# Optimization experiments

Hardware: AMD Instinct MI355X
Metric: run time of the kernel (lower is better)

Reference implementation:

```python
import jax, jax.numpy as jnp
import numpy as np

B, L = 4, 2048
D_MODEL = 1024
D_INNER = 2048      # expand * d_model
D_STATE = 16
D_CONV = 4
DT_RANK = 64        # ceil(d_model / 16)
EPS = 1e-5


def setup_inputs() -> dict:
    key = jax.random.key(0)
    ks = jax.random.split(key, 8)
    s = 0.02
    return {
        "x": jax.random.normal(ks[0], (B, L, D_MODEL), jnp.float32),
        "ln1_g": jnp.ones((D_MODEL,), jnp.float32),
        "ln1_b": jnp.zeros((D_MODEL,), jnp.float32),
        "ln2_g": jnp.ones((D_MODEL,), jnp.float32),
        "ln2_b": jnp.zeros((D_MODEL,), jnp.float32),
        "in_proj_w": jax.random.normal(ks[1], (D_MODEL, 2 * D_INNER), jnp.float32) * s,
        "conv_w": jax.random.normal(ks[2], (D_INNER, D_CONV), jnp.float32) * s,
        "conv_b": jnp.zeros((D_INNER,), jnp.float32),
        "x_proj_w": jax.random.normal(ks[3], (D_INNER, DT_RANK + 2 * D_STATE), jnp.float32) * s,
        "dt_proj_w": jax.random.normal(ks[4], (DT_RANK, D_INNER), jnp.float32) * s,
        # softplus^{-1}(0.01): mamba-style dt bias init
        "dt_proj_b": jnp.log(jnp.expm1(jnp.full((D_INNER,), 0.01, jnp.float32))),
        "A_log": jnp.log(jnp.broadcast_to(jnp.arange(1, D_STATE + 1, dtype=jnp.float32), (D_INNER, D_STATE))),
        "Dp": jnp.ones((D_INNER,), jnp.float32),
        "out_proj_w": jax.random.normal(ks[5], (D_INNER, D_MODEL), jnp.float32) * s,
        "mlp_w": jax.random.normal(ks[6], (D_MODEL, D_MODEL), jnp.float32) * s,
        "mlp_b": jnp.zeros((D_MODEL,), jnp.float32),
    }


def _layernorm(x, g, b):
    mu = jnp.mean(x, axis=-1, keepdims=True)
    var = jnp.mean(jnp.square(x - mu), axis=-1, keepdims=True)
    return (x - mu) * jax.lax.rsqrt(var + EPS) * g + b


def _mamba(x, in_proj_w, conv_w, conv_b, x_proj_w, dt_proj_w, dt_proj_b, A_log, Dp, out_proj_w):
    # x: (B, L, d_model)
    xz = x @ in_proj_w                       # (B, L, 2*d_inner)
    u, z = jnp.split(xz, 2, axis=-1)         # each (B, L, d_inner)

    # depthwise causal conv1d, kernel width D_CONV
    up = jnp.pad(u, ((0, 0), (D_CONV - 1, 0), (0, 0)))
    uc = conv_b
    for k in range(D_CONV):
        uc = uc + up[:, k:k + L, :] * conv_w[:, k]
    u = jax.nn.silu(uc)                      # (B, L, d_inner)

    dbc = u @ x_proj_w                       # (B, L, dt_rank + 2*d_state)
    dt = dbc[..., :DT_RANK]
    Bm = dbc[..., DT_RANK:DT_RANK + D_STATE]  # (B, L, d_state)
    Cm = dbc[..., DT_RANK + D_STATE:]         # (B, L, d_state)
    delta = jax.nn.softplus(dt @ dt_proj_w + dt_proj_b)  # (B, L, d_inner)
    A = -jnp.exp(A_log)                      # (d_inner, d_state)

    def step(h, inp):
        u_t, d_t, B_t, C_t = inp             # (B,d_inner),(B,d_inner),(B,d_state),(B,d_state)
        dA = jnp.exp(d_t[:, :, None] * A)    # (B, d_inner, d_state)
        h = dA * h + (d_t * u_t)[:, :, None] * B_t[:, None, :]
        y = jnp.einsum('bds,bs->bd', h, C_t)
        return h, y

    h0 = jnp.zeros((x.shape[0], D_INNER, D_STATE), x.dtype)
    xs = (u.transpose(1, 0, 2), delta.transpose(1, 0, 2),
          Bm.transpose(1, 0, 2), Cm.transpose(1, 0, 2))
    _, ys = jax.lax.scan(step, h0, xs)       # ys: (L, B, d_inner)
    y = ys.transpose(1, 0, 2) + u * Dp
    y = y * jax.nn.silu(z)
    return y @ out_proj_w                    # (B, L, d_model)


def reference(x, ln1_g, ln1_b, ln2_g, ln2_b, in_proj_w, conv_w, conv_b,
              x_proj_w, dt_proj_w, dt_proj_b, A_log, Dp, out_proj_w, mlp_w, mlp_b):
    h = _layernorm(x, ln1_g, ln1_b)
    h = _mamba(h, in_proj_w, conv_w, conv_b, x_proj_w, dt_proj_w, dt_proj_b,
               A_log, Dp, out_proj_w)
    # residual=False -> x = x_ssm; stage 2: Linear + GELU (exact erf)
    h2 = _layernorm(h, ln2_g, ln2_b)
    out = jax.nn.gelu(h2 @ mlp_w + mlp_b, approximate=False)
    return out
```

## Files before the change

### kernel.cpp

```cpp
#include <hip/hip_runtime.h>
#include <hip/hip_bf16.h>
#include <math.h>

#define BB 4
#define LL 2048
#define DM 1024
#define DI 2048
#define DS 16
#define DC 4
#define DTR 64

#define NCH 8
#define TC  (LL / NCH)

typedef __hip_bfloat16 bf16;
typedef unsigned int u32;
typedef unsigned short u16;
typedef u16 u16x8 __attribute__((ext_vector_type(8)));
typedef u16 u16x4 __attribute__((ext_vector_type(4)));
typedef short short8 __attribute__((ext_vector_type(8)));
typedef float f32x4 __attribute__((ext_vector_type(4)));

__device__ __forceinline__ float bfb2f(u16 b) { return __uint_as_float(((u32)b) << 16); }
__device__ __forceinline__ u16 f2bfb(float f) {
  bf16 h = __float2bfloat16(f);
  u16 r; __builtin_memcpy(&r, &h, 2); return r;
}

__device__ __forceinline__ float xld(const void* p, size_t i, bool isbf) {
  return isbf ? __bfloat162float(((const bf16*)p)[i]) : ((const float*)p)[i];
}
__device__ __forceinline__ bool probe_bf(const u32* probe) {
  return probe[0] == 0x3F803F80u;
}

__device__ __forceinline__ float softplus_f(float x) {
  return fmaxf(x, 0.f) + __logf(1.f + __expf(-fabsf(x)));
}
__device__ __forceinline__ float gelu_f(float x) {
  return 0.5f * x * (1.f + erff(x * 0.70710678118654752440f));
}
__device__ __forceinline__ float silu_f(float x) {
  return x * __builtin_amdgcn_rcpf(1.f + __expf(-x));
}

template<int PAT>
__device__ __forceinline__ float swz_xor(float v) {
  return __uint_as_float(
      (u32)__builtin_amdgcn_ds_swizzle((int)__float_as_uint(v), PAT));
}
template<int CTRL>
__device__ __forceinline__ float dpp_xchg(float v) {
  return __uint_as_float((u32)__builtin_amdgcn_update_dpp(
      0, (int)__float_as_uint(v), CTRL, 0xF, 0xF, true));
}

__device__ __forceinline__ float block_sum(float v, float* sm) {
  #pragma unroll
  for (int o = 32; o > 0; o >>= 1) v += __shfl_down(v, o, 64);
  int w = threadIdx.x >> 6;
  __syncthreads();
  if ((threadIdx.x & 63) == 0) sm[w] = v;
  __syncthreads();
  return sm[0] + sm[1] + sm[2] + sm[3];
}

template<bool EXT>
__global__ __launch_bounds__(256)
void ln_kernel(const void* __restrict__ X, const void* __restrict__ g,
               const void* __restrict__ bvec, bf16* __restrict__ Y,
               const u32* __restrict__ probe) {
  __shared__ float sm[4];
  bool isbf = probe_bf(probe);
  int row = blockIdx.x;
  int tid = threadIdx.x;
  size_t base = (size_t)row * DM;
  float v[4];
  float s = 0.f;
  #pragma unroll
  for (int i = 0; i < 4; i++) {
    int c = tid + 256 * i;
    v[i] = EXT ? xld(X, base + c, isbf) : ((const float*)X)[base + c];
    s += v[i];
  }
  float mu = block_sum(s, sm) * (1.f / DM);
  float vs = 0.f;
  #pragma unroll
  for (int i = 0; i < 4; i++) { float d = v[i] - mu; vs += d * d; }
  float var = block_sum(vs, sm) * (1.f / DM);
  float inv = rsqrtf(var + 1e-5f);
  bf16* yr = Y + base;
  #pragma unroll
  for (int i = 0; i < 4; i++) {
    int c = tid + 256 * i;
    yr[c] = __float2bfloat16((v[i] - mu) * inv * xld(g, c, isbf) + xld(bvec, c, isbf));
  }
}

__global__ __launch_bounds__(256)
void transpose_w(const void* __restrict__ W, u16* __restrict__ WT,
                 int K, int N, const u32* __restrict__ probe) {
  __shared__ u16 tile[32][33];
  bool isbf = probe_bf(probe);
  int c = threadIdx.x & 31;
  int r0 = threadIdx.x >> 5;
  int n0 = blockIdx.x * 32;
  int k0 = blockIdx.y * 32;
  #pragma unroll
  for (int rr = 0; rr < 32; rr += 8) {
    int r = r0 + rr;
    tile[r][c] = f2bfb(xld(W, (size_t)(k0 + r) * N + n0 + c, isbf));
  }
  __syncthreads();
  #pragma unroll
  for (int rr = 0; rr < 32; rr += 8) {
    int r = r0 + rr;
    WT[(size_t)(n0 + r) * K + k0 + c] = tile[c][r];
  }
}

__global__ __launch_bounds__(256)
void transpose_y(const u16* __restrict__ src, u16* __restrict__ dst) {
  __shared__ u16 tile[32][33];
  const size_t PER_B = (size_t)DI * LL;
  int b = blockIdx.z;
  int t0 = blockIdx.x * 32;
  int d0 = blockIdx.y * 32;
  int c = threadIdx.x & 31;
  int r0 = threadIdx.x >> 5;
  #pragma unroll
  for (int rr = 0; rr < 32; rr += 8) {
    int r = r0 + rr;
    tile[r][c] = src[b * PER_B + (size_t)(d0 + r) * LL + t0 + c];
  }
  __syncthreads();
  #pragma unroll
  for (int rr = 0; rr < 32; rr += 8) {
    int r = r0 + rr;
    dst[b * PER_B + (size_t)(t0 + r) * DI + d0 + c] = tile[c][r];
  }
}

template<int EPI>
__global__ __launch_bounds__(256)
void gemm_mfma(const u16* __restrict__ A, int lda,
               const u16* __restrict__ BT,
               const void* __restrict__ bias,
               void* __restrict__ C0, void* __restrict__ C1, void* __restrict__ C2,
               int N, int K, int ldc,
               const u32* __restrict__ probe) {
  __shared__ u16 As[128][40];
  __shared__ u16 Bs[128][40];
  bool isbf = probe_bf(probe);
  int tid = threadIdx.x;
  int wave = tid >> 6;
  int lane = tid & 63;
  int wm = wave >> 1, wn = wave & 1;
  int quad = lane >> 4;
  int l15 = lane & 15;
  int m0 = blockIdx.y * 128;
  int n0 = blockIdx.x * 128;

  f32x4 acc[4][4] = {};

  int sr = tid >> 2;
  int scc = tid & 3;

  for (int k0 = 0; k0 < K; k0 += 32) {
    *(u16x8*)(&As[sr][scc * 8]) =
        *(const u16x8*)(A + (size_t)(m0 + sr) * lda + k0 + scc * 8);
    *(u16x8*)(&As[64 + sr][scc * 8]) =
        *(const u16x8*)(A + (size_t)(m0 + 64 + sr) * lda + k0 + scc * 8);
    *(u16x8*)(&Bs[sr][scc * 8]) =
        *(const u16x8*)(BT + (size_t)(n0 + sr) * K + k0 + scc * 8);
    *(u16x8*)(&Bs[64 + sr][scc * 8]) =
        *(const u16x8*)(BT + (size_t)(n0 + 64 + sr) * K + k0 + scc * 8);
    __syncthreads();
    short8 af[4], bf[4];
    #pragma unroll
    for (int i = 0; i < 4; i++) {
      af[i] = *(const short8*)(&As[wm * 64 + i * 16 + l15][quad * 8]);
      bf[i] = *(const short8*)(&Bs[wn * 64 + i * 16 + l15][quad * 8]);
    }
    #pragma unroll
    for (int i = 0; i < 4; i++)
      #pragma unroll
      for (int j = 0; j < 4; j++)
        acc[i][j] = __builtin_amdgcn_mfma_f32_16x16x32_bf16(af[i], bf[j], acc[i][j], 0, 0, 0);
    __syncthreads();
  }

  #pragma unroll
  for (int i = 0; i < 4; i++) {
    int rb = m0 + wm * 64 + i * 16 + quad * 4;
    #pragma unroll
    for (int j = 0; j < 4; j++) {
      int c = n0 + wn * 64 + j * 16 + l15;
      if (EPI == 0) {
        #pragma unroll
        for (int r = 0; r < 4; r++)
          ((float*)C0)[(size_t)(rb + r) * ldc + c] = acc[i][j][r];
      } else if (EPI == 2) {
        float bv = xld(bias, c, isbf);
        #pragma unroll
        for (int r = 0; r < 4; r++) {
          float v = gelu_f(acc[i][j][r] + bv);
          if (isbf) ((bf16*)C0)[(size_t)(rb + r) * ldc + c] = __float2bfloat16(v);
          else      ((float*)C0)[(size_t)(rb + r) * ldc + c] = v;
        }
      } else if (EPI == 3) {
        int b = rb >> 11;
        int t = rb & (LL - 1);
        u16x4 pk;
        #pragma unroll
        for (int r = 0; r < 4; r++) pk[r] = f2bfb(acc[i][j][r]);
        u16* dst = (c < DI) ? (u16*)C0 : (u16*)C1;
        int cc = (c < DI) ? c : c - DI;
        *(u16x4*)(dst + ((size_t)b * DI + cc) * LL + t) = pk;
      } else {
        int b = rb >> 11;
        int t = rb & (LL - 1);
        if (c < DTR) {
          #pragma unroll
          for (int r = 0; r < 4; r++)
            ((float*)C0)[(size_t)(rb + r) * DTR + c] = acc[i][j][r];
        } else if (c < DTR + 2 * DS) {
          float* dst = (c < DTR + DS) ? (float*)C1 : (float*)C2;
          int s = (c < DTR + DS) ? c - DTR : c - DTR - DS;
          float* p = dst + (((size_t)b * (LL / 8) + (t >> 3)) * DS + s) * 8 + (t & 7);
          #pragma unroll
          for (int r = 0; r < 4; r++) p[r] = acc[i][j][r];
        }
      }
    }
  }
}

__global__ __launch_bounds__(256)
void gemm_dtproj(const float* __restrict__ A, int lda,
                 const void* __restrict__ Bw, int ldb,
                 const void* __restrict__ bias,
                 u16* __restrict__ C0, int N, int K,
                 const u32* __restrict__ probe) {
  __shared__ float As[16][65];
  __shared__ float Bs[16][65];
  bool isbf = probe_bf(probe);
  int tid = threadIdx.x;
  int tx = tid & 15, ty = tid >> 4;
  int m0 = blockIdx.y * 64;
  int n0 = blockIdx.x * 64;
  float acc[4][4] = {};
  int arow = tid >> 2;
  int akq = (tid & 3) * 4;
  int bk = tid >> 4;
  int bcq = (tid & 15) * 4;

  for (int k0 = 0; k0 < K; k0 += 16) {
    const float* ap = A + (size_t)(m0 + arow) * lda + k0 + akq;
    #pragma unroll
    for (int i = 0; i < 4; i++) As[akq + i][arow] = ap[i];
    size_t boff = (size_t)(k0 + bk) * ldb + n0 + bcq;
    #pragma unroll
    for (int j = 0; j < 4; j++) Bs[bk][bcq + j] = xld(Bw, boff + j, isbf);
    __syncthreads();
    #pragma unroll
    for (int k = 0; k < 16; k++) {
      float a4[4], b4[4];
      #pragma unroll
      for (int i = 0; i < 4; i++) a4[i] = As[k][ty + 16 * i];
      #pragma unroll
      for (int j = 0; j < 4; j++) b4[j] = Bs[k][tx + 16 * j];
      #pragma unroll
      for (int i = 0; i < 4; i++)
        #pragma unroll
        for (int j = 0; j < 4; j++)
          acc[i][j] = fmaf(a4[i], b4[j], acc[i][j]);
    }
    __syncthreads();
  }
  #pragma unroll
  for (int i = 0; i < 4; i++) {
    int r = m0 + ty + 16 * i;
    int t = r & (LL - 1);
    int b = r >> 11;
    #pragma unroll
    for (int j = 0; j < 4; j++) {
      int c = n0 + tx + 16 * j;
      float sv = softplus_f(acc[i][j] + xld(bias, c, isbf));
      C0[((size_t)b * DI + c) * LL + t] = f2bfb(sv);
    }
  }
}

__global__ __launch_bounds__(256)
void conv_kernel(const u16* __restrict__ uT, const void* __restrict__ cw,
                 const void* __restrict__ cb, u16* __restrict__ ucT,
                 const u32* __restrict__ probe) {
  bool isbf = probe_bf(probe);
  size_t pos = ((size_t)blockIdx.x * 256 + threadIdx.x) * 8;
  int t0 = (int)(pos & (LL - 1));
  int d = (int)((pos >> 11) & (DI - 1));
  float w0 = xld(cw, d * DC + 0, isbf);
  float w1 = xld(cw, d * DC + 1, isbf);
  float w2 = xld(cw, d * DC + 2, isbf);
  float w3 = xld(cw, d * DC + 3, isbf);
  float bias = xld(cb, d, isbf);
  u16x8 cur = *(const u16x8*)(uT + pos);
  float u[11];
  if (t0 > 0) {
    u16x4 prev = *(const u16x4*)(uT + pos - 4);
    u[0] = bfb2f(prev[1]); u[1] = bfb2f(prev[2]); u[2] = bfb2f(prev[3]);
  } else {
    u[0] = 0.f; u[1] = 0.f; u[2] = 0.f;
  }
  #pragma unroll
  for (int i = 0; i < 8; i++) u[3 + i] = bfb2f(cur[i]);
  u16x8 out;
  #pragma unroll
  for (int i = 0; i < 8; i++) {
    float acc = bias + w0 * u[i] + w1 * u[i + 1] + w2 * u[i + 2] + w3 * u[i + 3];
    out[i] = f2bfb(silu_f(acc));
  }
  *(u16x8*)(ucT + pos) = out;
}

__global__ __launch_bounds__(256)
void scan_fused(const u16* __restrict__ zT, u16* __restrict__ ucT,
                const u16* __restrict__ deltaT,
                const float* __restrict__ Bt, const float* __restrict__ Ct,
                const void* __restrict__ A_log, const void* __restrict__ Dp,
                const u32* __restrict__ probe) {
  __shared__ float sP[2][NCH][DS];
  __shared__ float sH[2][NCH][DS];
  bool isbf = probe_bf(probe);
  int tid = threadIdx.x;
  int s = tid & 15;
  int chunk = (tid >> 4) & (NCH - 1);
  int cl = tid >> 7;
  int chain = blockIdx.x * 2 + cl;
  int b = chain >> 11;
  int d = chain & (DI - 1);

  float a = -__expf(xld(A_log, d * DS + s, isbf));
  const u16* dl = deltaT + ((size_t)b * DI + d) * LL + chunk * TC;
  const u16* up = ucT    + ((size_t)b * DI + d) * LL + chunk * TC;
  const float* bp = Bt + (((size_t)b * (LL / 8) + (chunk * TC >> 3)) * DS + s) * 8;

  float P = 1.f, Q = 0.f;
  for (int t0 = 0; t0 < TC; t0 += 8) {
    u16x8 dt8 = *(const u16x8*)(dl + t0);
    u16x8 u8  = *(const u16x8*)(up + t0);
    float4 b4a = *(const float4*)(bp + t0 * 16);
    float4 b4b = *(const float4*)(bp + t0 * 16 + 4);
    float Bv[8] = {b4a.x, b4a.y, b4a.z, b4a.w, b4b.x, b4b.y, b4b.z, b4b.w};
    #pragma unroll
    for (int i = 0; i < 8; i++) {
      float dt = bfb2f(dt8[i]);
      float uv = bfb2f(u8[i]);
      float dA = __expf(dt * a);
      Q = fmaf(dA, Q, dt * uv * Bv[i]);
      P *= dA;
    }
  }
  sP[cl][chunk][s] = P;
  sH[cl][chunk][s] = Q;
  __syncthreads();
  if (tid < 32) {
    int ci = tid >> 4, ss = tid & 15;
    float carry = 0.f;
    #pragma unroll
    for (int c = 0; c < NCH; c++) {
      float nxt = sP[ci][c][ss] * carry + sH[ci][c][ss];
      sH[ci][c][ss] = carry;
      carry = nxt;
    }
  }
  __syncthreads();
  float h = sH[cl][chunk][s];

  float dp = xld(Dp, d, isbf);
  const float* cp = Ct + (((size_t)b * (LL / 8) + (chunk * TC >> 3)) * DS + s) * 8;
  const u16* zp = zT  + ((size_t)b * DI + d) * LL + chunk * TC;
  u16* upw = ucT      + ((size_t)b * DI + d) * LL + chunk * TC;
  bool k8 = (s & 8) != 0;
  bool k1 = (s & 1) != 0;
  bool k4 = (s & 4) != 0;
  int ei = ((s >> 3) & 1) * 4 + (s & 1) * 2 + ((s >> 2) & 1);
  bool estore = (s & 2) == 0;

  for (int t0 = 0; t0 < TC; t0 += 8) {
    u16x8 dt8 = *(const u16x8*)(dl + t0);
    u16x8 u8  = *(const u16x8*)(up + t0);
    float4 b4a = *(const float4*)(bp + t0 * 16);
    float4 b4b = *(const float4*)(bp + t0 * 16 + 4);
    float4 c4a = *(const float4*)(cp + t0 * 16);
    float4 c4b = *(const float4*)(cp + t0 * 16 + 4);
    float Bv[8] = {b4a.x, b4a.y, b4a.z, b4a.w, b4b.x, b4b.y, b4b.z, b4b.w};
    float Cv[8] = {c4a.x, c4a.y, c4a.z, c4a.w, c4b.x, c4b.y, c4b.z, c4b.w};
    float v[8];
    #pragma unroll
    for (int i = 0; i < 8; i++) {
      float dt = bfb2f(dt8[i]);
      float uv = bfb2f(u8[i]);
      float dA = __expf(dt * a);
      h = fmaf(dA, h, dt * uv * Bv[i]);
      v[i] = h * Cv[i];
    }
    float w4[4];
    #pragma unroll
    for (int j = 0; j < 4; j++) {
      float lo = v[j], hi = v[j + 4];
      float snd = k8 ? lo : hi;
      float kp  = k8 ? hi : lo;
      w4[j] = kp + dpp_xchg<0x128>(snd);
    }
    float w2[2];
    #pragma unroll
    for (int k = 0; k < 2; k++) {
      float lo = w4[k], hi = w4[k + 2];
      float snd = k1 ? lo : hi;
      float kp  = k1 ? hi : lo;
      w2[k] = kp + dpp_xchg<0xB1>(snd);
    }
    float y1;
    {
      float lo = w2[0], hi = w2[1];
      float snd = k4 ? lo : hi;
      float kp  = k4 ? hi : lo;
      y1 = kp + swz_xor<0x101F>(snd);
    }
    y1 += dpp_xchg<0x4E>(y1);
    int t = t0 + ei;
    float uvs = bfb2f(up[t]);
    float zvs = bfb2f(zp[t]);
    float val = fmaf(uvs, dp, y1) * silu_f(zvs);
    if (estore) upw[t] = f2bfb(val);
  }
}

extern "C" void kernel_launch(void* const* d_in, const int* in_sizes, int n_in,
                              void* d_out, int out_size, void* d_ws, size_t ws_size,
                              hipStream_t stream) {
  const void* x         = d_in[0];
  const u32*  probe     = (const u32*)d_in[1];
  const void* ln1_g     = d_in[1];
  const void* ln1_b     = d_in[2];
  const void* ln2_g     = d_in[3];
  const void* ln2_b     = d_in[4];
  const void* in_proj_w = d_in[5];
  const void* conv_w    = d_in[6];
  const void* conv_b    = d_in[7];
  const void* x_proj_w  = d_in[8];
  const void* dt_proj_w = d_in[9];
  const void* dt_proj_b = d_in[10];
  const void* A_log     = d_in[11];
  const void* Dp        = d_in[12];
  const void* out_proj_w= d_in[13];
  const void* mlp_w     = d_in[14];
  const void* mlp_b     = d_in[15];

  const size_t MB = 1024 * 1024;
  char* ws = (char*)d_ws;
  bf16*  h1       = (bf16*)(ws + 0);
  u16*   opwT     = (u16*)(ws + 0);
  bf16*  h2       = (bf16*)(ws + 0);
  u16*   xpwT     = (u16*)(ws + 4 * MB);
  u16*   uT       = (u16*)(ws + 16 * MB);
  u16*   uc2      = uT;
  u16*   deltaT   = uT;
  u16*   y        = uT;
  u16*   zT       = (u16*)(ws + 48 * MB);
  float* o        = (float*)(ws + 48 * MB);
  u16*   ipwT     = (u16*)(ws + 80 * MB);
  u16*   ucT      = (u16*)(ws + 80 * MB);
  u16*   mlpwT    = (u16*)(ws + 80 * MB);
  float* dbc_dt   = (float*)(ws + 112 * MB);
  float* Bt       = (float*)(ws + 114 * MB);
  float* Ct       = (float*)(ws + 114 * MB + 512 * 1024);

  transpose_w<<<dim3(4096 / 32, 1024 / 32), 256, 0, stream>>>(in_proj_w, ipwT, DM, 2 * DI, probe);
  ln_kernel<true><<<BB * LL, 256, 0, stream>>>(x, ln1_g, ln1_b, h1, probe);
  gemm_mfma<3><<<dim3(4096 / 128, 8192 / 128), 256, 0, stream>>>(
      (const u16*)h1, DM, ipwT, nullptr, uT, zT, nullptr, 2 * DI, DM, 0, probe);
  transpose_w<<<dim3(1024 / 32, 2048 / 32), 256, 0, stream>>>(out_proj_w, opwT, DI, DM, probe);
  conv_kernel<<<(BB * DI * LL / 8) / 256, 256, 0, stream>>>(uT, conv_w, conv_b, ucT, probe);
  transpose_w<<<dim3(96 / 32, 2048 / 32), 256, 0, stream>>>(x_proj_w, xpwT, DI, 96, probe);
  transpose_y<<<dim3(LL / 32, DI / 32, BB), 256, 0, stream>>>(ucT, uc2);
  gemm_mfma<4><<<dim3(1, 8192 / 128), 256, 0, stream>>>(
      uc2, DI, xpwT, nullptr, dbc_dt, Bt, Ct, 128, DI, 0, probe);
  gemm_dtproj<<<dim3(32, 128), 256, 0, stream>>>(dbc_dt, DTR, dt_proj_w, DI, dt_proj_b, deltaT, DI, DTR, probe);
  scan_fused<<<(BB * DI) / 2, 256, 0, stream>>>(
      zT, ucT, deltaT, Bt, Ct, A_log, Dp, probe);
  transpose_y<<<dim3(LL / 32, DI / 32, BB), 256, 0, stream>>>(ucT, y);
  gemm_mfma<0><<<dim3(1024 / 128, 8192 / 128), 256, 0, stream>>>(
      y, DI, opwT, nullptr, o, nullptr, nullptr, DM, DI, DM, probe);
  transpose_w<<<dim3(1024 / 32, 1024 / 32), 256, 0, stream>>>(mlp_w, mlpwT, DM, DM, probe);
  ln_kernel<false><<<BB * LL, 256, 0, stream>>>(o, ln2_g, ln2_b, h2, probe);
  gemm_mfma<2><<<dim3(1024 / 128, 8192 / 128), 256, 0, stream>>>(
      (const u16*)h2, DM, mlpwT, mlp_b, d_out, nullptr, nullptr, DM, DM, DM, probe);
}
```

Baseline: 695.2 us.

## Process two channels per thread in selective scan to reuse B/C loads

Each thread in the fused scan now handles two adjacent d_inner channels, using float2 vector math so the B and C loads are shared between them. The grid is halved to match and the shared carry arrays grow to four chains per block. This cuts redundant B/C memory traffic and may allow packed FP32 math, but it raises register pressure, halves the number of blocks available for latency hiding, and doubles the sequential work per thread.

```diff
diff --git a/kernel.cpp b/kernel.cpp
--- a/kernel.cpp
+++ b/kernel.cpp
@@ -20,6 +20,7 @@
 typedef u16 u16x4 __attribute__((ext_vector_type(4)));
 typedef short short8 __attribute__((ext_vector_type(8)));
 typedef float f32x4 __attribute__((ext_vector_type(4)));
+typedef float f32x2 __attribute__((ext_vector_type(2)));
 
 __device__ __forceinline__ float bfb2f(u16 b) { return __uint_as_float(((u32)b) << 16); }
 __device__ __forceinline__ u16 f2bfb(float f) {
@@ -53,6 +54,13 @@
 __device__ __forceinline__ float dpp_xchg(float v) {
   return __uint_as_float((u32)__builtin_amdgcn_update_dpp(
       0, (int)__float_as_uint(v), CTRL, 0xF, 0xF, true));
+}
+template<int CTRL>
+__device__ __forceinline__ f32x2 dpp_xchg2(f32x2 v) {
+  f32x2 r;
+  r.x = dpp_xchg<CTRL>(v.x);
+  r.y = dpp_xchg<CTRL>(v.y);
+  return r;
 }
 
 __device__ __forceinline__ float block_sum(float v, float* sm) {
@@ -330,42 +338,52 @@
                 const float* __restrict__ Bt, const float* __restrict__ Ct,
                 const void* __restrict__ A_log, const void* __restrict__ Dp,
                 const u32* __restrict__ probe) {
-  __shared__ float sP[2][NCH][DS];
-  __shared__ float sH[2][NCH][DS];
+  __shared__ float sP[4][NCH][DS];
+  __shared__ float sH[4][NCH][DS];
   bool isbf = probe_bf(probe);
   int tid = threadIdx.x;
   int s = tid & 15;
   int chunk = (tid >> 4) & (NCH - 1);
   int cl = tid >> 7;
-  int chain = blockIdx.x * 2 + cl;
-  int b = chain >> 11;
-  int d = chain & (DI - 1);
-
-  float a = -__expf(xld(A_log, d * DS + s, isbf));
-  const u16* dl = deltaT + ((size_t)b * DI + d) * LL + chunk * TC;
-  const u16* up = ucT    + ((size_t)b * DI + d) * LL + chunk * TC;
+  int chain0 = blockIdx.x * 4 + cl * 2;
+  int b = chain0 >> 11;
+  int d0 = chain0 & (DI - 1);
+
+  f32x2 a2;
+  a2.x = -__expf(xld(A_log, (size_t)d0 * DS + s, isbf));
+  a2.y = -__expf(xld(A_log, (size_t)(d0 + 1) * DS + s, isbf));
+  size_t base0 = ((size_t)b * DI + d0) * LL + chunk * TC;
+  const u16* dl0 = deltaT + base0;
+  const u16* dl1 = dl0 + LL;
+  const u16* up0 = ucT + base0;
+  const u16* up1 = up0 + LL;
   const float* bp = Bt + (((size_t)b * (LL / 8) + (chunk * TC >> 3)) * DS + s) * 8;
 
-  float P = 1.f, Q = 0.f;
+  f32x2 P = {1.f, 1.f}, Q = {0.f, 0.f};
   for (int t0 = 0; t0 < TC; t0 += 8) {
-    u16x8 dt8 = *(const u16x8*)(dl + t0);
-    u16x8 u8  = *(const u16x8*)(up + t0);
+    u16x8 dtA = *(const u16x8*)(dl0 + t0);
+    u16x8 dtB = *(const u16x8*)(dl1 + t0);
+    u16x8 uA  = *(const u16x8*)(up0 + t0);
+    u16x8 uB  = *(const u16x8*)(up1 + t0);
     float4 b4a = *(const float4*)(bp + t0 * 16);
     float4 b4b = *(const float4*)(bp + t0 * 16 + 4);
     float Bv[8] = {b4a.x, b4a.y, b4a.z, b4a.w, b4b.x, b4b.y, b4b.z, b4b.w};
     #pragma unroll
     for (int i = 0; i < 8; i++) {
-      float dt = bfb2f(dt8[i]);
-      float uv = bfb2f(u8[i]);
-      float dA = __expf(dt * a);
-      Q = fmaf(dA, Q, dt * uv * Bv[i]);
+      f32x2 dt; dt.x = bfb2f(dtA[i]); dt.y = bfb2f(dtB[i]);
+      f32x2 uv; uv.x = bfb2f(uA[i]);  uv.y = bfb2f(uB[i]);
+      f32x2 e = dt * a2;
+      f32x2 dA; dA.x = __expf(e.x); dA.y = __expf(e.y);
+      Q = dA * Q + dt * uv * Bv[i];
       P *= dA;
     }
   }
-  sP[cl][chunk][s] = P;
-  sH[cl][chunk][s] = Q;
+  sP[cl * 2 + 0][chunk][s] = P.x;
+  sP[cl * 2 + 1][chunk][s] = P.y;
+  sH[cl * 2 + 0][chunk][s] = Q.x;
+  sH[cl * 2 + 1][chunk][s] = Q.y;
   __syncthreads();
-  if (tid < 32) {
+  if (tid < 64) {
     int ci = tid >> 4, ss = tid & 15;
     float carry = 0.f;
     #pragma unroll
@@ -376,12 +394,16 @@
     }
   }
   __syncthreads();
-  float h = sH[cl][chunk][s];
-
-  float dp = xld(Dp, d, isbf);
+  f32x2 h;
+  h.x = sH[cl * 2 + 0][chunk][s];
+  h.y = sH[cl * 2 + 1][chunk][s];
+
+  f32x2 dp2; dp2.x = xld(Dp, d0, isbf); dp2.y = xld(Dp, d0 + 1, isbf);
   const float* cp = Ct + (((size_t)b * (LL / 8) + (chunk * TC >> 3)) * DS + s) * 8;
-  const u16* zp = zT  + ((size_t)b * DI + d) * LL + chunk * TC;
-  u16* upw = ucT      + ((size_t)b * DI + d) * LL + chunk * TC;
+  const u16* zp0 = zT + base0;
+  const u16* zp1 = zp0 + LL;
+  u16* uw0 = ucT + base0;
+  u16* uw1 = uw0 + LL;
   bool k8 = (s & 8) != 0;
   bool k1 = (s & 1) != 0;
   bool k4 = (s & 4) != 0;
@@ -389,52 +411,61 @@
   bool estore = (s & 2) == 0;
 
   for (int t0 = 0; t0 < TC; t0 += 8) {
-    u16x8 dt8 = *(const u16x8*)(dl + t0);
-    u16x8 u8  = *(const u16x8*)(up + t0);
+    u16x8 dtA = *(const u16x8*)(dl0 + t0);
+    u16x8 dtB = *(const u16x8*)(dl1 + t0);
+    u16x8 uA  = *(const u16x8*)(up0 + t0);
+    u16x8 uB  = *(const u16x8*)(up1 + t0);
     float4 b4a = *(const float4*)(bp + t0 * 16);
     float4 b4b = *(const float4*)(bp + t0 * 16 + 4);
     float4 c4a = *(const float4*)(cp + t0 * 16);
     float4 c4b = *(const float4*)(cp + t0 * 16 + 4);
     float Bv[8] = {b4a.x, b4a.y, b4a.z, b4a.w, b4b.x, b4b.y, b4b.z, b4b.w};
     float Cv[8] = {c4a.x, c4a.y, c4a.z, c4a.w, c4b.x, c4b.y, c4b.z, c4b.w};
-    float v[8];
+    f32x2 v[8];
     #pragma unroll
     for (int i = 0; i < 8; i++) {
-      float dt = bfb2f(dt8[i]);
-      float uv = bfb2f(u8[i]);
-      float dA = __expf(dt * a);
-      h = fmaf(dA, h, dt * uv * Bv[i]);
+      f32x2 dt; dt.x = bfb2f(dtA[i]); dt.y = bfb2f(dtB[i]);
+      f32x2 uv; uv.x = bfb2f(uA[i]);  uv.y = bfb2f(uB[i]);
+      f32x2 e = dt * a2;
+      f32x2 dA; dA.x = __expf(e.x); dA.y = __expf(e.y);
+      h = dA * h + dt * uv * Bv[i];
       v[i] = h * Cv[i];
     }
-    float w4[4];
+    f32x2 w4[4];
     #pragma unroll
     for (int j = 0; j < 4; j++) {
-      float lo = v[j], hi = v[j + 4];
-      float snd = k8 ? lo : hi;
-      float kp  = k8 ? hi : lo;
-      w4[j] = kp + dpp_xchg<0x128>(snd);
-    }
-    float w2[2];
+      f32x2 lo = v[j], hi = v[j + 4];
+      f32x2 snd = k8 ? lo : hi;
+      f32x2 kp  = k8 ? hi : lo;
+      w4[j] = kp + dpp_xchg2<0x128>(snd);
+    }
+    f32x2 w2[2];
     #pragma unroll
     for (int k = 0; k < 2; k++) {
-      float lo = w4[k], hi = w4[k + 2];
-      float snd = k1 ? lo : hi;
-      float kp  = k1 ? hi : lo;
-      w2[k] = kp + dpp_xchg<0xB1>(snd);
-    }
-    float y1;
+      f32x2 lo = w4[k], hi = w4[k + 2];
+      f32x2 snd = k1 ? lo : hi;
+      f32x2 kp  = k1 ? hi : lo;
+      w2[k] = kp + dpp_xchg2<0xB1>(snd);
+    }
+    f32x2 y1;
     {
-      float lo = w2[0], hi = w2[1];
-      float snd = k4 ? lo : hi;
-      float kp  = k4 ? hi : lo;
-      y1 = kp + swz_xor<0x101F>(snd);
-    }
-    y1 += dpp_xchg<0x4E>(y1);
+      f32x2 lo = w2[0], hi = w2[1];
+      f32x2 snd = k4 ? lo : hi;
+      f32x2 kp  = k4 ? hi : lo;
+      y1.x = kp.x + swz_xor<0x101F>(snd.x);
+      y1.y = kp.y + swz_xor<0x101F>(snd.y);
+    }
+    y1 += dpp_xchg2<0x4E>(y1);
     int t = t0 + ei;
-    float uvs = bfb2f(up[t]);
-    float zvs = bfb2f(zp[t]);
-    float val = fmaf(uvs, dp, y1) * silu_f(zvs);
-    if (estore) upw[t] = f2bfb(val);
+    f32x2 uvs; uvs.x = bfb2f(up0[t]); uvs.y = bfb2f(up1[t]);
+    f32x2 zvs; zvs.x = bfb2f(zp0[t]); zvs.y = bfb2f(zp1[t]);
+    f32x2 val = (uvs * dp2 + y1);
+    val.x *= silu_f(zvs.x);
+    val.y *= silu_f(zvs.y);
+    if (estore) {
+      uw0[t] = f2bfb(val.x);
+      uw1[t] = f2bfb(val.y);
+    }
   }
 }
 
@@ -489,7 +520,7 @@
   gemm_mfma<4><<<dim3(1, 8192 / 128), 256, 0, stream>>>(
       uc2, DI, xpwT, nullptr, dbc_dt, Bt, Ct, 128, DI, 0, probe);
   gemm_dtproj<<<dim3(32, 128), 256, 0, stream>>>(dbc_dt, DTR, dt_proj_w, DI, dt_proj_b, deltaT, DI, DTR, probe);
-  scan_fused<<<(BB * DI) / 2, 256, 0, stream>>>(
+  scan_fused<<<(BB * DI) / 4, 256, 0, stream>>>(
       zT, ucT, deltaT, Bt, Ct, A_log, Dp, probe);
   transpose_y<<<dim3(LL / 32, DI / 32, BB), 256, 0, stream>>>(ucT, y);
   gemm_mfma<0><<<dim3(1024 / 128, 8192 / 128), 256, 0, stream>>>(
```

Result: faster. 675.4 us (-2.8%).
